# Kernel tuning notes

Hardware: AMD Instinct MI355X
Metric: run time of the kernel (lower is better)

Reference implementation:

```python
import jax, jax.numpy as jnp
import numpy as np


def setup_inputs() -> dict:
    key = jax.random.key(0)
    k1, k2 = jax.random.split(key)
    B, C, H, W, D = 4, 32, 256, 512, 48
    h1 = jax.random.normal(k1, (B, C, H, W), dtype=jnp.float32)
    cost = jax.random.normal(k2, (B, D, H, W), dtype=jnp.float32)
    return {"h1": h1, "cost": cost}


def reference(h1, cost):
    # g2[b,c,h,w] = sum_d cost[b,d,h,w] * stop_grad(h1)[b,c,h,w+d]  for w+d < W
    # (original torch code detaches h1, so grads only flow through cost)
    B, C, H, W = h1.shape
    D = cost.shape[1]
    h1d = jax.lax.stop_gradient(h1)
    w_idx = jnp.arange(W)

    # scan over disparity levels; each step does a masked roll + fused MAC,
    # never materializing the [B,C,D,H,W] shifted stack.
    cost_d_major = jnp.moveaxis(cost, 1, 0)  # [D,B,H,W]

    def step(acc, xd):
        d, c_d = xd  # c_d: [B,H,W]
        valid = (w_idx < (W - d)).astype(h1.dtype)  # [W]; zero beyond W-d
        shifted = jnp.roll(h1d, -d, axis=-1) * valid  # h1[..., w+d], zero-padded
        acc = acc + c_d[:, None, :, :] * shifted  # broadcast over C
        return acc, None

    g2, _ = jax.lax.scan(step, jnp.zeros_like(h1), (jnp.arange(D), cost_d_major))
    return g2
```

## Files before the change

### kernel.cpp

```cpp
#include <hip/hip_runtime.h>


#define BB 4
#define CC 32
#define HH 256
#define WW 512
#define DDISP 48
#define HW (HH * WW)
#define TW 256
#define WROW 312
#define NT 256

__global__ __launch_bounds__(NT, 4)
void dense_warp_kernel(const float* __restrict__ h1,
                       const float* __restrict__ cost,
                       float* __restrict__ out)
{
    __shared__ float h1s[CC * WROW];

    const int blk    = blockIdx.x;
    const int wside  = blk & 1;
    const int h      = (blk >> 1) & (HH - 1);
    const int b      = blk >> 9;
    const int wstart = wside * TW;
    const int tid    = threadIdx.x;

    {
        const float* src = h1 + ((size_t)b * CC * HH + (size_t)h) * WW;
        for (int idx = tid; idx < CC * 78; idx += NT) {
            int r    = idx / 78;
            int q    = idx - r * 78;
            int col  = q << 2;
            int wsrc = wstart + col;
            float4 v = make_float4(0.f, 0.f, 0.f, 0.f);
            if (wsrc < WW) v = *(const float4*)(src + (size_t)r * HW + wsrc);
            *(float4*)(&h1s[r * WROW + col]) = v;
        }
    }
    __syncthreads();

    const int lane = tid & 63;
    const int wid  = tid >> 6;
    const int c0   = wid << 3;
    const int w0   = lane << 2;

    float acc[8][4];
#pragma unroll
    for (int c = 0; c < 8; ++c)
#pragma unroll
        for (int j = 0; j < 4; ++j) acc[c][j] = 0.f;

    float win[8][8];
    const float* lptr = &h1s[c0 * WROW + w0];
#pragma unroll
    for (int c = 0; c < 8; ++c) {
        float4 q0 = *(const float4*)(lptr + c * WROW);
        float4 q1 = *(const float4*)(lptr + c * WROW + 4);
        win[c][0] = q0.x; win[c][1] = q0.y; win[c][2] = q0.z; win[c][3] = q0.w;
        win[c][4] = q1.x; win[c][5] = q1.y; win[c][6] = q1.z; win[c][7] = q1.w;
    }

    const float* cp = cost + ((size_t)b * DDISP * HH + (size_t)h) * WW + wstart + w0;

    float cv[4][4];

#define LOADC(gofs) do {                                                       \
    _Pragma("unroll")                                                          \
    for (int dd = 0; dd < 4; ++dd) {                                           \
        float4 t = *(const float4*)(cp + (size_t)((gofs) + dd) * HW);          \
        cv[dd][0] = t.x; cv[dd][1] = t.y; cv[dd][2] = t.z; cv[dd][3] = t.w;    \
    }                                                                          \
} while (0)

#define DO_GROUP(P) do {                                                       \
    _Pragma("unroll")                                                          \
    for (int c = 0; c < 8; ++c) {                                              \
        _Pragma("unroll")                                                      \
        for (int dd = 0; dd < 4; ++dd) {                                       \
            _Pragma("unroll")                                                  \
            for (int j = 0; j < 4; ++j) {                                      \
                const int o    = dd + j;                             \
                const int slot = ((P) + (o >> 2)) & 1;                         \
                acc[c][j] += cv[dd][j] * win[c][slot * 4 + (o & 3)];           \
            }                                                                  \
        }                                                                      \
                        \
        float4 t = *(const float4*)(lptr + c * WROW + 8);                      \
        win[c][(P) * 4 + 0] = t.x; win[c][(P) * 4 + 1] = t.y;                  \
        win[c][(P) * 4 + 2] = t.z; win[c][(P) * 4 + 3] = t.w;                  \
    }                                                                          \
    lptr += 4;                                                                 \
} while (0)

    for (int ig = 0; ig < 6; ++ig) {
        LOADC(0);
        DO_GROUP(0);
        LOADC(4);
        DO_GROUP(1);
        cp += (size_t)8 * HW;
    }
#undef LOADC
#undef DO_GROUP

    float* outBase = out + ((size_t)b * CC * HH + (size_t)h) * WW + wstart + w0;
#pragma unroll
    for (int c = 0; c < 8; ++c) {
        float* op = outBase + (size_t)(c0 + c) * HW;
        *(float4*)op = make_float4(acc[c][0], acc[c][1], acc[c][2], acc[c][3]);
    }
}

extern "C" void kernel_launch(void* const* d_in, const int* in_sizes, int n_in,
                              void* d_out, int out_size, void* d_ws, size_t ws_size,
                              hipStream_t stream) {
    const float* h1   = (const float*)d_in[0];
    const float* cost = (const float*)d_in[1];
    float* out        = (float*)d_out;
    dim3 grid(BB * HH * 2);
    dense_warp_kernel<<<grid, NT, 0, stream>>>(h1, cost, out);
}
```

Before: 248.0 us.

## Triple-buffer cost loads in registers and prefetch before the shared-memory fill

```diff
diff --git a/kernel.cpp b/kernel.cpp
--- a/kernel.cpp
+++ b/kernel.cpp
@@ -25,6 +25,27 @@
     const int wstart = wside * TW;
     const int tid    = threadIdx.x;
 
+    const int lane = tid & 63;
+    const int wid  = tid >> 6;
+    const int c0   = wid << 3;
+    const int w0   = lane << 2;
+
+    const float* cp = cost + ((size_t)b * DDISP * HH + (size_t)h) * WW + wstart + w0;
+
+    float cv0[4][4], cv1[4][4], cv2[4][4];
+
+#define LOADCV(buf, g) do {                                                    \
+    _Pragma("unroll")                                                          \
+    for (int dd = 0; dd < 4; ++dd) {                                           \
+        float4 t = *(const float4*)(cp + (size_t)(4 * (g) + dd) * HW);         \
+        buf[dd][0] = t.x; buf[dd][1] = t.y;                                    \
+        buf[dd][2] = t.z; buf[dd][3] = t.w;                                    \
+    }                                                                          \
+} while (0)
+
+    LOADCV(cv0, 0);
+    LOADCV(cv1, 1);
+
     {
         const float* src = h1 + ((size_t)b * CC * HH + (size_t)h) * WW;
         for (int idx = tid; idx < CC * 78; idx += NT) {
@@ -39,67 +60,43 @@
     }
     __syncthreads();
 
-    const int lane = tid & 63;
-    const int wid  = tid >> 6;
-    const int c0   = wid << 3;
-    const int w0   = lane << 2;
-
     float acc[8][4];
 #pragma unroll
     for (int c = 0; c < 8; ++c)
 #pragma unroll
         for (int j = 0; j < 4; ++j) acc[c][j] = 0.f;
 
-    float win[8][8];
-    const float* lptr = &h1s[c0 * WROW + w0];
-#pragma unroll
-    for (int c = 0; c < 8; ++c) {
-        float4 q0 = *(const float4*)(lptr + c * WROW);
-        float4 q1 = *(const float4*)(lptr + c * WROW + 4);
-        win[c][0] = q0.x; win[c][1] = q0.y; win[c][2] = q0.z; win[c][3] = q0.w;
-        win[c][4] = q1.x; win[c][5] = q1.y; win[c][6] = q1.z; win[c][7] = q1.w;
-    }
+    const float* lbase = &h1s[c0 * WROW + w0];
 
-    const float* cp = cost + ((size_t)b * DDISP * HH + (size_t)h) * WW + wstart + w0;
-
-    float cv[4][4];
-
-#define LOADC(gofs) do {                                                       \
+#define DO_GROUP(buf, g) do {                                                  \
     _Pragma("unroll")                                                          \
-    for (int dd = 0; dd < 4; ++dd) {                                           \
-        float4 t = *(const float4*)(cp + (size_t)((gofs) + dd) * HW);          \
-        cv[dd][0] = t.x; cv[dd][1] = t.y; cv[dd][2] = t.z; cv[dd][3] = t.w;    \
+    for (int c = 0; c < 8; ++c) {                                              \
+        const float* lp = lbase + c * WROW + 4 * (g);                          \
+        float4 q0 = *(const float4*)(lp);                                      \
+        float4 q1 = *(const float4*)(lp + 4);                                  \
+        float srcv[8] = { q0.x, q0.y, q0.z, q0.w, q1.x, q1.y, q1.z, q1.w };    \
+        _Pragma("unroll")                                                      \
+        for (int dd = 0; dd < 4; ++dd)                                         \
+            _Pragma("unroll")                                                  \
+            for (int j = 0; j < 4; ++j)                                        \
+                acc[c][j] += buf[dd][j] * srcv[dd + j];                        \
     }                                                                          \
 } while (0)
 
-#define DO_GROUP(P) do {                                                       \
-    _Pragma("unroll")                                                          \
-    for (int c = 0; c < 8; ++c) {                                              \
-        _Pragma("unroll")                                                      \
-        for (int dd = 0; dd < 4; ++dd) {                                       \
-            _Pragma("unroll")                                                  \
-            for (int j = 0; j < 4; ++j) {                                      \
-                const int o    = dd + j;                             \
-                const int slot = ((P) + (o >> 2)) & 1;                         \
-                acc[c][j] += cv[dd][j] * win[c][slot * 4 + (o & 3)];           \
-            }                                                                  \
-        }                                                                      \
-                        \
-        float4 t = *(const float4*)(lptr + c * WROW + 8);                      \
-        win[c][(P) * 4 + 0] = t.x; win[c][(P) * 4 + 1] = t.y;                  \
-        win[c][(P) * 4 + 2] = t.z; win[c][(P) * 4 + 3] = t.w;                  \
-    }                                                                          \
-    lptr += 4;                                                                 \
-} while (0)
+    LOADCV(cv2,  2);  DO_GROUP(cv0,  0);
+    LOADCV(cv0,  3);  DO_GROUP(cv1,  1);
+    LOADCV(cv1,  4);  DO_GROUP(cv2,  2);
+    LOADCV(cv2,  5);  DO_GROUP(cv0,  3);
+    LOADCV(cv0,  6);  DO_GROUP(cv1,  4);
+    LOADCV(cv1,  7);  DO_GROUP(cv2,  5);
+    LOADCV(cv2,  8);  DO_GROUP(cv0,  6);
+    LOADCV(cv0,  9);  DO_GROUP(cv1,  7);
+    LOADCV(cv1, 10);  DO_GROUP(cv2,  8);
+    LOADCV(cv2, 11);  DO_GROUP(cv0,  9);
+                      DO_GROUP(cv1, 10);
+                      DO_GROUP(cv2, 11);
 
-    for (int ig = 0; ig < 6; ++ig) {
-        LOADC(0);
-        DO_GROUP(0);
-        LOADC(4);
-        DO_GROUP(1);
-        cp += (size_t)8 * HW;
-    }
-#undef LOADC
+#undef LOADCV
 #undef DO_GROUP
 
     float* outBase = out + ((size_t)b * CC * HH + (size_t)h) * WW + wstart + w0;
```

Measured after the change: 277.4 us. 1.12x slower.

## Split channels across two blocks and drop register sliding window

Applied to the files above, without the earlier changes.

```diff
diff --git a/kernel.cpp b/kernel.cpp
--- a/kernel.cpp
+++ b/kernel.cpp
@@ -3,6 +3,7 @@
 
 #define BB 4
 #define CC 32
+#define CHB 16
 #define HH 256
 #define WW 512
 #define DDISP 48
@@ -11,23 +12,24 @@
 #define WROW 312
 #define NT 256
 
-__global__ __launch_bounds__(NT, 4)
+__global__ __launch_bounds__(NT, 8)
 void dense_warp_kernel(const float* __restrict__ h1,
                        const float* __restrict__ cost,
                        float* __restrict__ out)
 {
-    __shared__ float h1s[CC * WROW];
+    __shared__ float h1s[CHB * WROW];
 
     const int blk    = blockIdx.x;
     const int wside  = blk & 1;
     const int h      = (blk >> 1) & (HH - 1);
-    const int b      = blk >> 9;
+    const int chalf  = (blk >> 9) & 1;
+    const int b      = blk >> 10;
     const int wstart = wside * TW;
     const int tid    = threadIdx.x;
 
     {
-        const float* src = h1 + ((size_t)b * CC * HH + (size_t)h) * WW;
-        for (int idx = tid; idx < CC * 78; idx += NT) {
+        const float* src = h1 + (((size_t)b * CC + chalf * CHB) * HH + (size_t)h) * WW;
+        for (int idx = tid; idx < CHB * 78; idx += NT) {
             int r    = idx / 78;
             int q    = idx - r * 78;
             int col  = q << 2;
@@ -41,70 +43,47 @@
 
     const int lane = tid & 63;
     const int wid  = tid >> 6;
-    const int c0   = wid << 3;
+    const int c0   = wid << 2;
     const int w0   = lane << 2;
 
-    float acc[8][4];
+    float acc[4][4];
 #pragma unroll
-    for (int c = 0; c < 8; ++c)
+    for (int c = 0; c < 4; ++c)
 #pragma unroll
         for (int j = 0; j < 4; ++j) acc[c][j] = 0.f;
 
-    float win[8][8];
-    const float* lptr = &h1s[c0 * WROW + w0];
+    const float* lbase = &h1s[c0 * WROW + w0];
+    const float* cpg   = cost + ((size_t)b * DDISP * HH + (size_t)h) * WW + wstart + w0;
+
+#pragma unroll 1
+    for (int g = 0; g < 12; ++g) {
+        float cv[4][4];
 #pragma unroll
-    for (int c = 0; c < 8; ++c) {
-        float4 q0 = *(const float4*)(lptr + c * WROW);
-        float4 q1 = *(const float4*)(lptr + c * WROW + 4);
-        win[c][0] = q0.x; win[c][1] = q0.y; win[c][2] = q0.z; win[c][3] = q0.w;
-        win[c][4] = q1.x; win[c][5] = q1.y; win[c][6] = q1.z; win[c][7] = q1.w;
+        for (int dd = 0; dd < 4; ++dd) {
+            float4 t = *(const float4*)(cpg + (size_t)dd * HW);
+            cv[dd][0] = t.x; cv[dd][1] = t.y; cv[dd][2] = t.z; cv[dd][3] = t.w;
+        }
+        cpg += (size_t)4 * HW;
+
+#pragma unroll
+        for (int c = 0; c < 4; ++c) {
+            const float* lp = lbase + c * WROW;
+            float4 q0 = *(const float4*)(lp);
+            float4 q1 = *(const float4*)(lp + 4);
+            float srcv[8] = { q0.x, q0.y, q0.z, q0.w, q1.x, q1.y, q1.z, q1.w };
+#pragma unroll
+            for (int dd = 0; dd < 4; ++dd)
+#pragma unroll
+                for (int j = 0; j < 4; ++j)
+                    acc[c][j] += cv[dd][j] * srcv[dd + j];
+        }
+        lbase += 4;
     }
 
-    const float* cp = cost + ((size_t)b * DDISP * HH + (size_t)h) * WW + wstart + w0;
-
-    float cv[4][4];
-
-#define LOADC(gofs) do {                                                       \
-    _Pragma("unroll")                                                          \
-    for (int dd = 0; dd < 4; ++dd) {                                           \
-        float4 t = *(const float4*)(cp + (size_t)((gofs) + dd) * HW);          \
-        cv[dd][0] = t.x; cv[dd][1] = t.y; cv[dd][2] = t.z; cv[dd][3] = t.w;    \
-    }                                                                          \
-} while (0)
-
-#define DO_GROUP(P) do {                                                       \
-    _Pragma("unroll")                                                          \
-    for (int c = 0; c < 8; ++c) {                                              \
-        _Pragma("unroll")                                                      \
-        for (int dd = 0; dd < 4; ++dd) {                                       \
-            _Pragma("unroll")                                                  \
-            for (int j = 0; j < 4; ++j) {                                      \
-                const int o    = dd + j;                             \
-                const int slot = ((P) + (o >> 2)) & 1;                         \
-                acc[c][j] += cv[dd][j] * win[c][slot * 4 + (o & 3)];           \
-            }                                                                  \
-        }                                                                      \
-                        \
-        float4 t = *(const float4*)(lptr + c * WROW + 8);                      \
-        win[c][(P) * 4 + 0] = t.x; win[c][(P) * 4 + 1] = t.y;                  \
-        win[c][(P) * 4 + 2] = t.z; win[c][(P) * 4 + 3] = t.w;                  \
-    }                                                                          \
-    lptr += 4;                                                                 \
-} while (0)
-
-    for (int ig = 0; ig < 6; ++ig) {
-        LOADC(0);
-        DO_GROUP(0);
-        LOADC(4);
-        DO_GROUP(1);
-        cp += (size_t)8 * HW;
-    }
-#undef LOADC
-#undef DO_GROUP
-
-    float* outBase = out + ((size_t)b * CC * HH + (size_t)h) * WW + wstart + w0;
+    float* outBase = out + (((size_t)b * CC + chalf * CHB) * HH + (size_t)h) * WW
+                     + wstart + w0;
 #pragma unroll
-    for (int c = 0; c < 8; ++c) {
+    for (int c = 0; c < 4; ++c) {
         float* op = outBase + (size_t)(c0 + c) * HW;
         *(float4*)op = make_float4(acc[c][0], acc[c][1], acc[c][2], acc[c][3]);
     }
@@ -116,6 +95,6 @@
     const float* h1   = (const float*)d_in[0];
     const float* cost = (const float*)d_in[1];
     float* out        = (float*)d_out;
-    dim3 grid(BB * HH * 2);
+    dim3 grid(BB * HH * 2 * 2);
     dense_warp_kernel<<<grid, NT, 0, stream>>>(h1, cost, out);
 }
```

After: 242.9 us. 2.0% less time.
